# Optimization experiments

Measured on AMD Instinct MI355X. Metric: run time of the kernel, lower is better.

The kernel has to match this reference:

```python
import jax, jax.numpy as jnp
import numpy as np

N_NODES = 20000
N_EDGES = 400000
B = 4            # number of edge_attr tensors in the Python loop (batch of graphs)
NODE_DIM = 256   # == hidden_dim (required: forward feeds raw x into edge_fc)
EDGE_DIM = 16
HIDDEN = 256
OUT_DIM = 128


def setup_inputs() -> dict:
    key = jax.random.key(0)
    ks = jax.random.split(key, 6)
    x = jax.random.normal(ks[0], (N_NODES, NODE_DIM), dtype=jnp.float32)
    edge_index = jax.random.randint(ks[1], (2, N_EDGES), 0, N_NODES, dtype=jnp.int64)
    edge_attrs = jax.random.normal(ks[2], (B, N_EDGES, EDGE_DIM), dtype=jnp.float32)
    fan_in = 2 * HIDDEN + EDGE_DIM  # edge_fc in_features
    W_edge = jax.random.normal(ks[3], (fan_in, HIDDEN), dtype=jnp.float32) / np.sqrt(fan_in).astype(np.float32)
    b_edge = jnp.zeros((HIDDEN,), dtype=jnp.float32)
    W_graph = jax.random.normal(ks[4], (HIDDEN, OUT_DIM), dtype=jnp.float32) / np.sqrt(HIDDEN).astype(np.float32)
    b_graph = jnp.zeros((OUT_DIM,), dtype=jnp.float32)
    return {"x": x, "edge_index": edge_index, "edge_attrs": edge_attrs,
            "W_edge": W_edge, "b_edge": b_edge, "W_graph": W_graph, "b_graph": b_graph}


def reference(x, edge_index, edge_attrs, W_edge, b_edge, W_graph, b_graph):
    # Original: for each edge_attr in edge_attrs:
    #   relu(cat([x[src], x[dst], edge_attr]) @ W_edge + b).mean(0) @ W_graph + b_graph
    # Equivalent: split W_edge by the concat blocks; the (src,dst) contribution is
    # shared across the batch, so compute it once and broadcast.
    D = x.shape[1]
    W_src, W_dst, W_attr = W_edge[:D], W_edge[D:2 * D], W_edge[2 * D:]
    src = x[edge_index[0]]                      # [E, D] gather
    dst = x[edge_index[1]]                      # [E, D] gather
    base = src @ W_src + dst @ W_dst + b_edge   # [E, H]
    h = jax.nn.relu(base[None, :, :] + jnp.einsum('bea,ah->beh', edge_attrs, W_attr))  # [B, E, H]
    graph_feat = h.mean(axis=1)                 # [B, H] mean pool over edges
    return graph_feat @ W_graph + b_graph       # [B, OUT]
```

## Files before the change

kernel.cpp:

```cpp
#include <hip/hip_runtime.h>

#define N_NODES 20000
#define N_EDGES 400000
#define NODE_DIM 256
#define HIDDEN 256
#define OUT_DIM 128
#define PROJ_BLOCKS 628
#define CONV_BLOCKS 1024
#define EDGE_GRID 1250

typedef __attribute__((ext_vector_type(8))) short short8;
typedef __attribute__((ext_vector_type(4))) float f32x4;

__device__ inline unsigned short f2bf(float f) {
  union { float f; unsigned u; } v; v.f = f;
  unsigned r = (v.u + 0x7FFFu + ((v.u >> 16) & 1u)) >> 16;
  return (unsigned short)r;
}

__global__ __launch_bounds__(256) void proj_mfma(
    const float* __restrict__ x, const float* __restrict__ We,
    const float* __restrict__ be, unsigned short* __restrict__ C,
    float* __restrict__ partial, const float* __restrict__ attrs,
    unsigned short* __restrict__ attrs_bf) {
  const int tid = threadIdx.x;
  if (blockIdx.x >= PROJ_BLOCKS) {
    const int nt = CONV_BLOCKS * 256;
    const int total4 = 4 * N_EDGES * 16 / 4;
    for (int i = (blockIdx.x - PROJ_BLOCKS) * 256 + tid; i < total4; i += nt) {
      float4 v = ((const float4*)attrs)[i];
      ushort4 o;
      o.x = f2bf(v.x); o.y = f2bf(v.y); o.z = f2bf(v.z); o.w = f2bf(v.w);
      ((ushort4*)attrs_bf)[i] = o;
    }
    return;
  }
  if (blockIdx.x == 0) {
    for (int i = tid; i < 4 * HIDDEN; i += 256) partial[i] = 0.f;
  }
  const int bm = blockIdx.x >> 2;
  const int bn = blockIdx.x & 3;
  const int row0 = bm * 128;
  const int col0 = bn * 128;
  const int half = col0 >> 8;
  const int ncol0 = col0 & 255;
  const int lane = tid & 63, wave = tid >> 6;
  const int q = lane >> 4, c = lane & 15;
  const int wm = wave >> 1, wn = wave & 1;

  __shared__ unsigned short As[128][32];
  __shared__ unsigned short Bs[128][32];

  f32x4 acc[4][4];
#pragma unroll
  for (int i = 0; i < 4; ++i)
#pragma unroll
    for (int t = 0; t < 4; ++t) acc[i][t] = (f32x4){0.f, 0.f, 0.f, 0.f};

  const int ar = tid >> 1;
  const int ak = (tid & 1) * 16;
  const int bk = tid >> 3;
  const int bn0 = (tid & 7) * 16;

  for (int k0 = 0; k0 < NODE_DIM; k0 += 32) {
    {
      const int r = row0 + ar;
      short8 t0, t1;
      if (r < N_NODES) {
        const float4* src = (const float4*)&x[(size_t)r * NODE_DIM + k0 + ak];
        float4 f0 = src[0], f1 = src[1], f2 = src[2], f3 = src[3];
        t0[0]=f2bf(f0.x); t0[1]=f2bf(f0.y); t0[2]=f2bf(f0.z); t0[3]=f2bf(f0.w);
        t0[4]=f2bf(f1.x); t0[5]=f2bf(f1.y); t0[6]=f2bf(f1.z); t0[7]=f2bf(f1.w);
        t1[0]=f2bf(f2.x); t1[1]=f2bf(f2.y); t1[2]=f2bf(f2.z); t1[3]=f2bf(f2.w);
        t1[4]=f2bf(f3.x); t1[5]=f2bf(f3.y); t1[6]=f2bf(f3.z); t1[7]=f2bf(f3.w);
      } else {
#pragma unroll
        for (int j = 0; j < 8; ++j) { t0[j] = 0; t1[j] = 0; }
      }
      *(short8*)&As[ar][ak] = t0;
      *(short8*)&As[ar][ak + 8] = t1;
    }
    {
      const float4* src = (const float4*)&We[(size_t)(half * 256 + k0 + bk) * HIDDEN + ncol0 + bn0];
#pragma unroll
      for (int v = 0; v < 4; ++v) {
        float4 f = src[v];
        Bs[bn0 + v * 4 + 0][bk] = f2bf(f.x);
        Bs[bn0 + v * 4 + 1][bk] = f2bf(f.y);
        Bs[bn0 + v * 4 + 2][bk] = f2bf(f.z);
        Bs[bn0 + v * 4 + 3][bk] = f2bf(f.w);
      }
    }
    __syncthreads();
    short8 Af[4], Bf[4];
#pragma unroll
    for (int i = 0; i < 4; ++i) Af[i] = *(const short8*)&As[wm * 64 + i * 16 + c][q * 8];
#pragma unroll
    for (int t = 0; t < 4; ++t) Bf[t] = *(const short8*)&Bs[wn * 64 + t * 16 + c][q * 8];
#pragma unroll
    for (int i = 0; i < 4; ++i)
#pragma unroll
      for (int t = 0; t < 4; ++t)
        acc[i][t] = __builtin_amdgcn_mfma_f32_16x16x32_bf16(Af[i], Bf[t], acc[i][t], 0, 0, 0);
    __syncthreads();
  }

  float biasv[4] = {0.f, 0.f, 0.f, 0.f};
  const int nbase = ncol0 + wn * 64;
  if (half) {
#pragma unroll
    for (int t = 0; t < 4; ++t) biasv[t] = be[nbase + t * 16 + c];
  }
#pragma unroll
  for (int i = 0; i < 4; ++i) {
#pragma unroll
    for (int r = 0; r < 4; ++r) {
      const int node = row0 + wm * 64 + i * 16 + q * 4 + r;
      if (node < N_NODES) {
        ushort4 o;
        o.x = f2bf(acc[i][0][r] + biasv[0]);
        o.y = f2bf(acc[i][1][r] + biasv[1]);
        o.z = f2bf(acc[i][2][r] + biasv[2]);
        o.w = f2bf(acc[i][3][r] + biasv[3]);
        *(ushort4*)&C[(size_t)node * 512 + half * 256 + nbase + c * 4] = o;
      }
    }
  }
}

template <bool PRE>
__global__ __launch_bounds__(256) void edge_mfma(
    const unsigned short* __restrict__ C, const int* __restrict__ ei,
    const float* __restrict__ attrs_f, const unsigned short* __restrict__ attrs_b,
    const float* __restrict__ We, float* __restrict__ partial) {
  const int tid = threadIdx.x;
  const int lane = tid & 63, wave = tid >> 6;
  const int q = lane >> 4, c = lane & 15;
  const int hb = wave * 64;

  short8 Bf[4];
#pragma unroll
  for (int t = 0; t < 4; ++t) {
    short8 bf;
#pragma unroll
    for (int j = 0; j < 8; ++j) {
      int k = q * 8 + j;
      float w = (k < 16) ? We[(size_t)(512 + k) * HIDDEN + hb + t * 16 + c] : 0.0f;
      bf[j] = (short)f2bf(w);
    }
    Bf[t] = bf;
  }

  f32x4 accs[4];
#pragma unroll
  for (int b = 0; b < 4; ++b) accs[b] = (f32x4){0.f, 0.f, 0.f, 0.f};

  const f32x4 zero4 = {0.f, 0.f, 0.f, 0.f};
  const int ngroups = N_EDGES / 16;
  for (int g = blockIdx.x; g < ngroups; g += gridDim.x) {
    const int e0 = g * 16;
    const int4 ns4 = *(const int4*)&ei[e0 + q * 4];
    const int4 nd4 = *(const int4*)&ei[N_EDGES + e0 + q * 4];

    short8 Af[4];
    if (PRE) {
      if (q < 2) {
#pragma unroll
        for (int b = 0; b < 4; ++b)
          Af[b] = *(const short8*)&attrs_b[((size_t)b * N_EDGES + e0 + c) * 16 + q * 8];
      } else {
        short8 z;
#pragma unroll
        for (int j = 0; j < 8; ++j) z[j] = 0;
#pragma unroll
        for (int b = 0; b < 4; ++b) Af[b] = z;
      }
    } else {
      if (q < 2) {
#pragma unroll
        for (int b = 0; b < 4; ++b) {
          const size_t off = ((size_t)b * N_EDGES + e0 + c) * 16 + q * 8;
          const float4 a0 = *(const float4*)&attrs_f[off];
          const float4 a1 = *(const float4*)&attrs_f[off + 4];
          short8 af;
          af[0]=f2bf(a0.x); af[1]=f2bf(a0.y); af[2]=f2bf(a0.z); af[3]=f2bf(a0.w);
          af[4]=f2bf(a1.x); af[5]=f2bf(a1.y); af[6]=f2bf(a1.z); af[7]=f2bf(a1.w);
          Af[b] = af;
        }
      } else {
        short8 z;
#pragma unroll
        for (int j = 0; j < 8; ++j) z[j] = 0;
#pragma unroll
        for (int b = 0; b < 4; ++b) Af[b] = z;
      }
    }

    f32x4 base4[4];
    {
      const int nn[4] = {ns4.x, ns4.y, ns4.z, ns4.w};
      const int dd[4] = {nd4.x, nd4.y, nd4.z, nd4.w};
#pragma unroll
      for (int r = 0; r < 4; ++r) {
        const uint2 s = *(const uint2*)&C[(size_t)nn[r] * 512 + hb + c * 4];
        const uint2 d = *(const uint2*)&C[(size_t)dd[r] * 512 + 256 + hb + c * 4];
        base4[0][r] = __uint_as_float(s.x << 16) + __uint_as_float(d.x << 16);
        base4[1][r] = __uint_as_float(s.x & 0xFFFF0000u) + __uint_as_float(d.x & 0xFFFF0000u);
        base4[2][r] = __uint_as_float(s.y << 16) + __uint_as_float(d.y << 16);
        base4[3][r] = __uint_as_float(s.y & 0xFFFF0000u) + __uint_as_float(d.y & 0xFFFF0000u);
      }
    }

#pragma unroll
    for (int b = 0; b < 4; ++b) {
#pragma unroll
      for (int t = 0; t < 4; ++t) {
        f32x4 S = __builtin_amdgcn_mfma_f32_16x16x32_bf16(Af[b], Bf[t], zero4, 0, 0, 0);
        f32x4 u = S + base4[t];
        u[0] = fmaxf(u[0], 0.f); u[1] = fmaxf(u[1], 0.f);
        u[2] = fmaxf(u[2], 0.f); u[3] = fmaxf(u[3], 0.f);
        accs[b][t] += (u[0] + u[1]) + (u[2] + u[3]);
      }
    }
  }

#pragma unroll
  for (int b = 0; b < 4; ++b)
#pragma unroll
    for (int t = 0; t < 4; ++t) {
      float v = accs[b][t];
      v += __shfl_xor(v, 16, 64);
      v += __shfl_xor(v, 32, 64);
      if (q == 0) atomicAdd(&partial[b * HIDDEN + hb + t * 16 + c], v);
    }
}

__global__ __launch_bounds__(256) void graph_out(
    const float* __restrict__ partial, const float* __restrict__ Wg,
    const float* __restrict__ bg, float* __restrict__ out) {
  const int o = blockIdx.x;
  const int hh = threadIdx.x;
  const int lane = hh & 63, wave = hh >> 6;
  const float w = Wg[(size_t)hh * OUT_DIM + o];
  float v[4];
#pragma unroll
  for (int b = 0; b < 4; ++b) v[b] = partial[b * HIDDEN + hh] * w;
#pragma unroll
  for (int off = 32; off >= 1; off >>= 1)
#pragma unroll
    for (int b = 0; b < 4; ++b) v[b] += __shfl_down(v[b], off, 64);
  __shared__ float red[4][4];
  if (lane == 0)
#pragma unroll
    for (int b = 0; b < 4; ++b) red[wave][b] = v[b];
  __syncthreads();
  if (hh < 4) {
    float s = red[0][hh] + red[1][hh] + red[2][hh] + red[3][hh];
    out[hh * OUT_DIM + o] = s * (1.0f / (float)N_EDGES) + bg[o];
  }
}

extern "C" void kernel_launch(void* const* d_in, const int* in_sizes, int n_in,
                              void* d_out, int out_size, void* d_ws, size_t ws_size,
                              hipStream_t stream) {
  const float* x  = (const float*)d_in[0];
  const int*   ei = (const int*)d_in[1];
  const float* ea = (const float*)d_in[2];
  const float* We = (const float*)d_in[3];
  const float* be = (const float*)d_in[4];
  const float* Wg = (const float*)d_in[5];
  const float* bg = (const float*)d_in[6];
  float* out = (float*)d_out;

  const size_t C_bytes = (size_t)N_NODES * 512 * 2;
  const size_t A_bytes = (size_t)4 * N_EDGES * 16 * 2;
  unsigned short* C = (unsigned short*)d_ws;
  const bool pre = ws_size >= C_bytes + A_bytes + 4096;
  unsigned short* attrs_bf = pre ? (unsigned short*)((char*)d_ws + C_bytes) : nullptr;
  float* partial = (float*)((char*)d_ws + (pre ? C_bytes + A_bytes : C_bytes));

  const int grid1 = pre ? PROJ_BLOCKS + CONV_BLOCKS : PROJ_BLOCKS;
  proj_mfma<<<grid1, 256, 0, stream>>>(x, We, be, C, partial, ea, attrs_bf);
  if (pre)
    edge_mfma<true><<<EDGE_GRID, 256, 0, stream>>>(C, ei, nullptr, attrs_bf, We, partial);
  else
    edge_mfma<false><<<EDGE_GRID, 256, 0, stream>>>(C, ei, ea, nullptr, We, partial);
  graph_out<<<128, 256, 0, stream>>>(partial, Wg, bg, out);
}
```

Measured before the change: 274.7 us.

## Spread edge atomics over partial copies, pad LDS rows, enlarge edge grid

The edge kernel's final atomicAdds now go to one of eight replicated partial buffers chosen by block index, and graph_out sums those copies. This cuts contention on the single 4x256 accumulator. The edge grid grows from 1250 to 3125 blocks, and the projection GEMM's LDS tiles get padded rows (stride 40) with a new B-load mapping that writes short8 vectors instead of scattered 2-byte stores. In exchange there is more workspace, the zeroing covers more memory, and the B loads are now strided scalar global reads.

```diff
diff --git a/kernel.cpp b/kernel.cpp
--- a/kernel.cpp
+++ b/kernel.cpp
@@ -7,7 +7,9 @@
 #define OUT_DIM 128
 #define PROJ_BLOCKS 628
 #define CONV_BLOCKS 1024
-#define EDGE_GRID 1250
+#define EDGE_GRID 3125
+#define NPART 8
+#define ROWP 40
 
 typedef __attribute__((ext_vector_type(8))) short short8;
 typedef __attribute__((ext_vector_type(4))) float f32x4;
@@ -36,7 +38,7 @@
     return;
   }
   if (blockIdx.x == 0) {
-    for (int i = tid; i < 4 * HIDDEN; i += 256) partial[i] = 0.f;
+    for (int i = tid; i < NPART * 4 * HIDDEN; i += 256) partial[i] = 0.f;
   }
   const int bm = blockIdx.x >> 2;
   const int bn = blockIdx.x & 3;
@@ -48,8 +50,8 @@
   const int q = lane >> 4, c = lane & 15;
   const int wm = wave >> 1, wn = wave & 1;
 
-  __shared__ unsigned short As[128][32];
-  __shared__ unsigned short Bs[128][32];
+  __shared__ unsigned short As[128 * ROWP];
+  __shared__ unsigned short Bs[128 * ROWP];
 
   f32x4 acc[4][4];
 #pragma unroll
@@ -59,8 +61,6 @@
 
   const int ar = tid >> 1;
   const int ak = (tid & 1) * 16;
-  const int bk = tid >> 3;
-  const int bn0 = (tid & 7) * 16;
 
   for (int k0 = 0; k0 < NODE_DIM; k0 += 32) {
     {
@@ -77,26 +77,31 @@
 #pragma unroll
         for (int j = 0; j < 8; ++j) { t0[j] = 0; t1[j] = 0; }
       }
-      *(short8*)&As[ar][ak] = t0;
-      *(short8*)&As[ar][ak + 8] = t1;
+      *(short8*)&As[ar * ROWP + ak] = t0;
+      *(short8*)&As[ar * ROWP + ak + 8] = t1;
     }
     {
-      const float4* src = (const float4*)&We[(size_t)(half * 256 + k0 + bk) * HIDDEN + ncol0 + bn0];
-#pragma unroll
-      for (int v = 0; v < 4; ++v) {
-        float4 f = src[v];
-        Bs[bn0 + v * 4 + 0][bk] = f2bf(f.x);
-        Bs[bn0 + v * 4 + 1][bk] = f2bf(f.y);
-        Bs[bn0 + v * 4 + 2][bk] = f2bf(f.z);
-        Bs[bn0 + v * 4 + 3][bk] = f2bf(f.w);
+#pragma unroll
+      for (int s = 0; s < 2; ++s) {
+        const int tau = tid + 256 * s;
+        const int kp = ((tau >> 6) & 3) * 8;
+        const int n  = (tau & 63) + ((tau >> 8) << 6);
+        short8 bb;
+#pragma unroll
+        for (int j = 0; j < 8; ++j)
+          bb[j] = (short)f2bf(
+              We[(size_t)(half * 256 + k0 + kp + j) * HIDDEN + ncol0 + n]);
+        *(short8*)&Bs[n * ROWP + kp] = bb;
       }
     }
     __syncthreads();
     short8 Af[4], Bf[4];
 #pragma unroll
-    for (int i = 0; i < 4; ++i) Af[i] = *(const short8*)&As[wm * 64 + i * 16 + c][q * 8];
-#pragma unroll
-    for (int t = 0; t < 4; ++t) Bf[t] = *(const short8*)&Bs[wn * 64 + t * 16 + c][q * 8];
+    for (int i = 0; i < 4; ++i)
+      Af[i] = *(const short8*)&As[(wm * 64 + i * 16 + c) * ROWP + q * 8];
+#pragma unroll
+    for (int t = 0; t < 4; ++t)
+      Bf[t] = *(const short8*)&Bs[(wn * 64 + t * 16 + c) * ROWP + q * 8];
 #pragma unroll
     for (int i = 0; i < 4; ++i)
 #pragma unroll
@@ -224,6 +229,7 @@
     }
   }
 
+  float* pp = partial + (size_t)(blockIdx.x & (NPART - 1)) * (4 * HIDDEN);
 #pragma unroll
   for (int b = 0; b < 4; ++b)
 #pragma unroll
@@ -231,7 +237,7 @@
       float v = accs[b][t];
       v += __shfl_xor(v, 16, 64);
       v += __shfl_xor(v, 32, 64);
-      if (q == 0) atomicAdd(&partial[b * HIDDEN + hb + t * 16 + c], v);
+      if (q == 0) atomicAdd(&pp[b * HIDDEN + hb + t * 16 + c], v);
     }
 }
 
@@ -244,7 +250,12 @@
   const float w = Wg[(size_t)hh * OUT_DIM + o];
   float v[4];
 #pragma unroll
-  for (int b = 0; b < 4; ++b) v[b] = partial[b * HIDDEN + hh] * w;
+  for (int b = 0; b < 4; ++b) {
+    float s = 0.f;
+#pragma unroll
+    for (int k = 0; k < NPART; ++k) s += partial[k * 4 * HIDDEN + b * HIDDEN + hh];
+    v[b] = s * w;
+  }
 #pragma unroll
   for (int off = 32; off >= 1; off >>= 1)
 #pragma unroll
@@ -274,8 +285,9 @@
 
   const size_t C_bytes = (size_t)N_NODES * 512 * 2;
   const size_t A_bytes = (size_t)4 * N_EDGES * 16 * 2;
+  const size_t P_bytes = (size_t)NPART * 4 * HIDDEN * 4;
   unsigned short* C = (unsigned short*)d_ws;
-  const bool pre = ws_size >= C_bytes + A_bytes + 4096;
+  const bool pre = ws_size >= C_bytes + A_bytes + P_bytes + 4096;
   unsigned short* attrs_bf = pre ? (unsigned short*)((char*)d_ws + C_bytes) : nullptr;
   float* partial = (float*)((char*)d_ws + (pre ? C_bytes + A_bytes : C_bytes));
 
```

Result: faster. 268.6 us (-2.2%).
